# Kernel tuning notes

Measured on AMD Instinct MI355X. Metric: run time of the kernel, lower is better.

The kernel has to match this reference:

```python
import jax, jax.numpy as jnp
import numpy as np

N_NODES = 50000
N_EDGES = 1600000
SLOPE = 0.01  # torch leaky_relu default negative_slope


def _lrelu(x):
    return jnp.where(x >= 0, x, SLOPE * x)


def _graph_conv(x, edge_index, w_rel, b_rel, w_root):
    # PyG GraphConv (aggr='add'): out_i = W_rel @ sum_{j->i} x_j + b_rel + W_root @ x_i
    src, dst = edge_index[0], edge_index[1]
    agg = jax.ops.segment_sum(x[src], dst, num_segments=x.shape[0])  # [N, F_in]
    return agg @ w_rel.T + b_rel + x @ w_root.T


def setup_inputs() -> dict:
    key = jax.random.key(0)
    ks = jax.random.split(key, 12)

    def glorot(k, shape):
        fan_in = shape[-1]
        return jax.random.normal(k, shape, dtype=jnp.float32) / np.sqrt(fan_in)

    x = jax.random.normal(ks[0], (N_NODES, 2048), dtype=jnp.float32)
    edge_index = jax.random.randint(ks[1], (2, N_EDGES), 0, N_NODES, dtype=jnp.int64)

    return {
        "x": x,
        "edge_index": edge_index,
        "lin1_w": glorot(ks[2], (128, 2048)),
        "lin1_b": jnp.zeros((128,), jnp.float32),
        "conv1_w_rel": glorot(ks[3], (64, 128)),
        "conv1_b_rel": jnp.zeros((64,), jnp.float32),
        "conv1_w_root": glorot(ks[4], (64, 128)),
        "conv4_w_rel": glorot(ks[5], (32, 64)),
        "conv4_b_rel": jnp.zeros((32,), jnp.float32),
        "conv4_w_root": glorot(ks[6], (32, 64)),
        "pos_w": glorot(ks[7], (3, 32)),
        "pos_b": jnp.zeros((3,), jnp.float32),
    }


def reference(x, edge_index, lin1_w, lin1_b, conv1_w_rel, conv1_b_rel,
              conv1_w_root, conv4_w_rel, conv4_b_rel, conv4_w_root,
              pos_w, pos_b):
    # dropout layers are identity at inference
    h = _lrelu(x @ lin1_w.T + lin1_b)                                  # [N, 128]
    h = _lrelu(_graph_conv(h, edge_index, conv1_w_rel, conv1_b_rel, conv1_w_root))  # [N, 64]
    h = _lrelu(_graph_conv(h, edge_index, conv4_w_rel, conv4_b_rel, conv4_w_root))  # [N, 32]
    position = h @ pos_w.T + pos_b                                     # [N, 3]
    return position
```

## Files before the change

kernel.cpp:

```cpp
#include <hip/hip_runtime.h>

#define N_NODES 50000
#define N_EDGES 1600000

typedef __attribute__((ext_vector_type(4))) float f32x4;
typedef __attribute__((ext_vector_type(8))) short bf16x8;
typedef unsigned short u16;

__device__ __forceinline__ float lrelu(float x) { return x >= 0.f ? x : 0.01f * x; }

__device__ __forceinline__ u16 f2bf(float f) {
    union { float f; unsigned u; } v; v.f = f;
    unsigned u = v.u;
    u += 0x7fffu + ((u >> 16) & 1u);
    return (u16)(u >> 16);
}

__device__ __forceinline__ float bf2f(u16 v) {
    union { unsigned u; float f; } x; x.u = ((unsigned)v) << 16; return x.f;
}

__device__ __forceinline__ bf16x8 cvt8(float4 a, float4 b) {
    bf16x8 r;
    r[0] = (short)f2bf(a.x); r[1] = (short)f2bf(a.y);
    r[2] = (short)f2bf(a.z); r[3] = (short)f2bf(a.w);
    r[4] = (short)f2bf(b.x); r[5] = (short)f2bf(b.y);
    r[6] = (short)f2bf(b.z); r[7] = (short)f2bf(b.w);
    return r;
}

__device__ __forceinline__ void gload_lds16(const void* g, void* l) {
    __builtin_amdgcn_global_load_lds(
        (const __attribute__((address_space(1))) void*)g,
        (__attribute__((address_space(3))) void*)l, 16, 0, 0);
}

__launch_bounds__(256)
__global__ void k_wprep1(const float* __restrict__ W, u16* __restrict__ Wf)
{
    int i = blockIdx.x * 256 + threadIdx.x;
    int e = i & 7, lane = (i >> 3) & 63, nf = (i >> 9) & 7, ks = i >> 12;
    int n = nf * 16 + (lane & 15);
    int k = ks * 32 + 8 * (lane >> 4) + e;
    Wf[i] = f2bf(W[(size_t)n * 2048 + k]);
}

__launch_bounds__(256)
__global__ void k_wprep2(const float* __restrict__ Wrel, const float* __restrict__ Wroot,
                         u16* __restrict__ Wf)
{
    int i = blockIdx.x * 256 + threadIdx.x;
    int e = i & 7, lane = (i >> 3) & 63, nf = (i >> 9) & 7, ks = i >> 12;
    int n = nf * 16 + (lane & 15);
    int k = ks * 32 + 8 * (lane >> 4) + e;
    float v = (n < 64) ? Wrel[(size_t)n * 128 + k] : Wroot[(size_t)(n - 64) * 128 + k];
    Wf[i] = f2bf(v);
}

__launch_bounds__(256)
__global__ void k_wprep3(const float* __restrict__ Wrel, const float* __restrict__ Wroot,
                         u16* __restrict__ Wf)
{
    int i = blockIdx.x * 256 + threadIdx.x;
    int e = i & 7, lane = (i >> 3) & 63, nf = (i >> 9) & 3, ks = i >> 11;
    int n = nf * 16 + (lane & 15);
    int k = ks * 32 + 8 * (lane >> 4) + e;
    float v = (n < 32) ? Wrel[(size_t)n * 64 + k] : Wroot[(size_t)(n - 32) * 64 + k];
    Wf[i] = f2bf(v);
}

__device__ __forceinline__ void stage_lin1(const float* __restrict__ X,
                                           const u16* __restrict__ Wf,
                                           char* Abuf, char* Bbuf,
                                           int m0, int s, int t)
{
    const int wave = t >> 6;
#pragma unroll
    for (int r = 0; r < 4; r++) {
        int row = r * 16 + (t >> 4);
        int grow = m0 + row; if (grow >= N_NODES) grow = 0;
        int bcol = ((t & 15) * 16) ^ ((row & 7) << 5);
        const float* src = X + (size_t)grow * 2048 + s * 64 + (bcol >> 2);
        gload_lds16(src, Abuf + r * 4096 + wave * 1024);
    }
#pragma unroll
    for (int r = 0; r < 4; r++) {
        const u16* src = Wf + (size_t)s * 8192 + ((size_t)(r * 256 + t)) * 8;
        gload_lds16(src, Bbuf + r * 4096 + wave * 1024);
    }
}

__launch_bounds__(256, 2)
__global__ void k_lin1s(const float* __restrict__ X, const u16* __restrict__ Wf,
                        const float* __restrict__ Bv, u16* __restrict__ H)
{
    __shared__ __align__(16) char As[2][16384];
    __shared__ __align__(16) char Bs[2][16384];

    const int t = threadIdx.x, wave = t >> 6, lane = t & 63;
    const int lrow = lane & 15, lgrp = lane >> 4;
    const int m0 = blockIdx.x * 64;
    const int myrow = wave * 16 + lrow;

    f32x4 acc[8];
#pragma unroll
    for (int i = 0; i < 8; i++) acc[i] = (f32x4)0.f;

    stage_lin1(X, Wf, As[0], Bs[0], m0, 0, t);
    __syncthreads();

    for (int s = 0; s < 32; s++) {
        const int cur = s & 1;
        if (s < 31) stage_lin1(X, Wf, As[cur ^ 1], Bs[cur ^ 1], m0, s + 1, t);

#pragma unroll
        for (int ksub = 0; ksub < 2; ksub++) {
            const int xr = (ksub * 128 + lgrp * 32) ^ ((myrow & 7) << 5);
            const float4* ar = (const float4*)(As[cur] + myrow * 256 + xr);
            float4 a0 = ar[0], a1 = ar[1];
            bf16x8 af = cvt8(a0, a1);
            const char* bb = Bs[cur] + ksub * 8192 + lane * 16;
#pragma unroll
            for (int nf = 0; nf < 8; nf++) {
                bf16x8 bf = *(const bf16x8*)(bb + nf * 1024);
                acc[nf] = __builtin_amdgcn_mfma_f32_16x16x32_bf16(af, bf, acc[nf], 0, 0, 0);
            }
        }
        __syncthreads();
    }

    const int rbase = m0 + wave * 16 + lgrp * 4;
#pragma unroll
    for (int nf = 0; nf < 8; nf++) {
        const int col = nf * 16 + lrow;
        const float bias = Bv[col];
#pragma unroll
        for (int r = 0; r < 4; r++) {
            const int row = rbase + r;
            if (row < N_NODES)
                H[(size_t)row * 128 + col] = f2bf(lrelu(acc[nf][r] + bias));
        }
    }
}

__launch_bounds__(256, 2)
__global__ void k_dualf1(const u16* __restrict__ Hb, const u16* __restrict__ Wf,
                         const float* __restrict__ brel,
                         u16* __restrict__ t1, float* __restrict__ acc1)
{
    const int t = threadIdx.x, wave = t >> 6, lane = t & 63;
    const int lrow = lane & 15, lgrp = lane >> 4;
    const int arow = blockIdx.x * 64 + wave * 16 + lrow;
    const u16* ap = Hb + (size_t)(arow < N_NODES ? arow : 0) * 128 + 8 * lgrp;
    const u16* bp = Wf + lane * 8;

    f32x4 acc[8];
#pragma unroll
    for (int i = 0; i < 8; i++) acc[i] = (f32x4)0.f;

    bf16x8 a0 = *(const bf16x8*)(ap + 0);
    bf16x8 a1 = *(const bf16x8*)(ap + 32);
    bf16x8 a2 = *(const bf16x8*)(ap + 64);
    bf16x8 a3 = *(const bf16x8*)(ap + 96);
    bf16x8 af[4] = {a0, a1, a2, a3};

#pragma unroll
    for (int ks = 0; ks < 4; ks++) {
        const u16* b = bp + ks * 4096;
        bf16x8 a = af[ks];
#pragma unroll
        for (int nf = 0; nf < 8; nf++) {
            bf16x8 bf = *(const bf16x8*)(b + nf * 512);
            acc[nf] = __builtin_amdgcn_mfma_f32_16x16x32_bf16(a, bf, acc[nf], 0, 0, 0);
        }
    }

    const int rbase = blockIdx.x * 64 + wave * 16 + lgrp * 4;
#pragma unroll
    for (int nf = 0; nf < 8; nf++) {
        const int col = nf * 16 + lrow;
#pragma unroll
        for (int r = 0; r < 4; r++) {
            const int row = rbase + r;
            if (row < N_NODES) {
                if (col < 64) t1[(size_t)row * 64 + col] = f2bf(acc[nf][r]);
                else          acc1[(size_t)row * 64 + (col - 64)] = acc[nf][r] + brel[col - 64];
            }
        }
    }
}

__launch_bounds__(256, 2)
__global__ void k_dualf2(const float* __restrict__ A, const u16* __restrict__ Wf,
                         const float* __restrict__ brel,
                         u16* __restrict__ t2, float* __restrict__ acc2)
{
    const int t = threadIdx.x, wave = t >> 6, lane = t & 63;
    const int lrow = lane & 15, lgrp = lane >> 4;
    const int arow = blockIdx.x * 64 + wave * 16 + lrow;
    const float* ap = A + (size_t)(arow < N_NODES ? arow : 0) * 64 + 8 * lgrp;
    const u16* bp = Wf + lane * 8;

    float4 a00 = *(const float4*)(ap + 0);
    float4 a01 = *(const float4*)(ap + 4);
    float4 a10 = *(const float4*)(ap + 32);
    float4 a11 = *(const float4*)(ap + 36);

    f32x4 acc[4];
#pragma unroll
    for (int i = 0; i < 4; i++) acc[i] = (f32x4)0.f;

    a00.x = lrelu(a00.x); a00.y = lrelu(a00.y); a00.z = lrelu(a00.z); a00.w = lrelu(a00.w);
    a01.x = lrelu(a01.x); a01.y = lrelu(a01.y); a01.z = lrelu(a01.z); a01.w = lrelu(a01.w);
    bf16x8 af0 = cvt8(a00, a01);
    a10.x = lrelu(a10.x); a10.y = lrelu(a10.y); a10.z = lrelu(a10.z); a10.w = lrelu(a10.w);
    a11.x = lrelu(a11.x); a11.y = lrelu(a11.y); a11.z = lrelu(a11.z); a11.w = lrelu(a11.w);
    bf16x8 af1 = cvt8(a10, a11);

#pragma unroll
    for (int nf = 0; nf < 4; nf++) {
        bf16x8 b0 = *(const bf16x8*)(bp + nf * 512);
        bf16x8 b1 = *(const bf16x8*)(bp + 2048 + nf * 512);
        acc[nf] = __builtin_amdgcn_mfma_f32_16x16x32_bf16(af0, b0, acc[nf], 0, 0, 0);
        acc[nf] = __builtin_amdgcn_mfma_f32_16x16x32_bf16(af1, b1, acc[nf], 0, 0, 0);
    }

    const int rbase = blockIdx.x * 64 + wave * 16 + lgrp * 4;
#pragma unroll
    for (int nf = 0; nf < 4; nf++) {
        const int col = nf * 16 + lrow;
#pragma unroll
        for (int r = 0; r < 4; r++) {
            const int row = rbase + r;
            if (row < N_NODES) {
                if (col < 32) t2[(size_t)row * 32 + col] = f2bf(acc[nf][r]);
                else          acc2[(size_t)row * 32 + (col - 32)] = acc[nf][r] + brel[col - 32];
            }
        }
    }
}

__launch_bounds__(256)
__global__ void k_zero(int* __restrict__ p, int n)
{
    int i = blockIdx.x * 256 + threadIdx.x;
    if (i < n) p[i] = 0;
}

__launch_bounds__(256)
__global__ void k_hist(const int* __restrict__ ei, int* __restrict__ deg)
{
    const int stride = gridDim.x * 256;
    for (int e = blockIdx.x * 256 + threadIdx.x; e < N_EDGES; e += stride)
        atomicAdd(deg + ei[N_EDGES + e], 1);
}

__launch_bounds__(256)
__global__ void k_scan1(const int* __restrict__ deg, int* __restrict__ tmp,
                        int* __restrict__ bsum)
{
    __shared__ int sm[256];
    const int tid = threadIdx.x;
    const int i = blockIdx.x * 256 + tid;
    int d = (i < N_NODES) ? deg[i] : 0;
    sm[tid] = d;
    __syncthreads();
#pragma unroll
    for (int off = 1; off < 256; off <<= 1) {
        int v = (tid >= off) ? sm[tid - off] : 0;
        __syncthreads();
        sm[tid] += v;
        __syncthreads();
    }
    if (i < N_NODES) tmp[i] = sm[tid];
    if (tid == 255) bsum[blockIdx.x] = sm[255];
}

__launch_bounds__(256)
__global__ void k_scan2p(const int* __restrict__ bsum, int* __restrict__ boff, int nb)
{
    __shared__ int sm[256];
    const int tid = threadIdx.x;
    int v = (tid < nb) ? bsum[tid] : 0;
    sm[tid] = v;
    __syncthreads();
#pragma unroll
    for (int off = 1; off < 256; off <<= 1) {
        int u = (tid >= off) ? sm[tid - off] : 0;
        __syncthreads();
        sm[tid] += u;
        __syncthreads();
    }
    if (tid < nb) boff[tid] = sm[tid] - v;
}

__launch_bounds__(256)
__global__ void k_scan3(const int* __restrict__ tmp, const int* __restrict__ boff,
                        const int* __restrict__ deg, int* __restrict__ ro,
                        int* __restrict__ cur)
{
    const int i = blockIdx.x * 256 + threadIdx.x;
    if (i < N_NODES) {
        int incl = tmp[i] + boff[i >> 8];
        ro[i + 1] = incl;
        cur[i] = incl - deg[i];
    }
    if (i == 0) ro[0] = 0;
}

__launch_bounds__(256)
__global__ void k_fill(const int* __restrict__ ei, int* __restrict__ cur,
                       int* __restrict__ csr)
{
    const int stride = gridDim.x * 256;
    for (int e = blockIdx.x * 256 + threadIdx.x; e < N_EDGES; e += stride) {
        const int dst = ei[N_EDGES + e];
        const int p = atomicAdd(cur + dst, 1);
        csr[p] = ei[e];
    }
}

__launch_bounds__(256)
__global__ void k_gather64(const int* __restrict__ ro, const int* __restrict__ csr,
                           const u16* __restrict__ t, float* __restrict__ acc)
{
    const int wid = (blockIdx.x << 2) | (threadIdx.x >> 6);
    if (wid >= N_NODES) return;
    const int lane = threadIdx.x & 63;
    const int s = ro[wid], e = ro[wid + 1];
    float a = acc[(size_t)wid * 64 + lane];
    int i = s;
    for (; i + 8 <= e; i += 8) {
        int s0 = csr[i], s1 = csr[i + 1], s2 = csr[i + 2], s3 = csr[i + 3];
        int s4 = csr[i + 4], s5 = csr[i + 5], s6 = csr[i + 6], s7 = csr[i + 7];
        u16 v0 = t[(size_t)s0 * 64 + lane], v1 = t[(size_t)s1 * 64 + lane];
        u16 v2 = t[(size_t)s2 * 64 + lane], v3 = t[(size_t)s3 * 64 + lane];
        u16 v4 = t[(size_t)s4 * 64 + lane], v5 = t[(size_t)s5 * 64 + lane];
        u16 v6 = t[(size_t)s6 * 64 + lane], v7 = t[(size_t)s7 * 64 + lane];
        a += bf2f(v0); a += bf2f(v1); a += bf2f(v2); a += bf2f(v3);
        a += bf2f(v4); a += bf2f(v5); a += bf2f(v6); a += bf2f(v7);
    }
    for (; i < e; ++i) a += bf2f(t[(size_t)csr[i] * 64 + lane]);
    acc[(size_t)wid * 64 + lane] = a;
}

__launch_bounds__(256)
__global__ void k_gpos(const int* __restrict__ ro, const int* __restrict__ csr,
                       const u16* __restrict__ t, const float* __restrict__ acc2,
                       const float* __restrict__ PW, const float* __restrict__ PB,
                       float* __restrict__ out)
{
    const int wid = (blockIdx.x << 2) | (threadIdx.x >> 6);
    if (wid >= N_NODES) return;
    const int lane = threadIdx.x & 63;
    const int half = lane >> 5, f = lane & 31;
    const int s = ro[wid], e = ro[wid + 1];
    float a = 0.f;
    int i = s;
    for (; i + 8 <= e; i += 8) {
        int s0 = csr[i + half], s1 = csr[i + 2 + half];
        int s2 = csr[i + 4 + half], s3 = csr[i + 6 + half];
        u16 v0 = t[(size_t)s0 * 32 + f], v1 = t[(size_t)s1 * 32 + f];
        u16 v2 = t[(size_t)s2 * 32 + f], v3 = t[(size_t)s3 * 32 + f];
        a += bf2f(v0); a += bf2f(v1); a += bf2f(v2); a += bf2f(v3);
    }
    for (; i < e; i += 2) {
        int idx = i + half;
        if (idx < e) a += bf2f(t[(size_t)csr[idx] * 32 + f]);
    }
    a += __shfl_xor(a, 32, 64);

    float v = lrelu(acc2[(size_t)wid * 32 + f] + a);
    float p0 = v * PW[f], p1 = v * PW[32 + f], p2 = v * PW[64 + f];
#pragma unroll
    for (int off = 16; off >= 1; off >>= 1) {
        p0 += __shfl_xor(p0, off, 64);
        p1 += __shfl_xor(p1, off, 64);
        p2 += __shfl_xor(p2, off, 64);
    }
    if (lane == 0) {
        out[(size_t)wid * 3 + 0] = p0 + PB[0];
        out[(size_t)wid * 3 + 1] = p1 + PB[1];
        out[(size_t)wid * 3 + 2] = p2 + PB[2];
    }
}

extern "C" void kernel_launch(void* const* d_in, const int* in_sizes, int n_in,
                              void* d_out, int out_size, void* d_ws, size_t ws_size,
                              hipStream_t stream)
{
    const float* x        = (const float*)d_in[0];
    const int*   ei       = (const int*)d_in[1];
    const float* lin1_w   = (const float*)d_in[2];
    const float* lin1_b   = (const float*)d_in[3];
    const float* c1_wrel  = (const float*)d_in[4];
    const float* c1_brel  = (const float*)d_in[5];
    const float* c1_wroot = (const float*)d_in[6];
    const float* c4_wrel  = (const float*)d_in[7];
    const float* c4_brel  = (const float*)d_in[8];
    const float* c4_wroot = (const float*)d_in[9];
    const float* pos_w    = (const float*)d_in[10];
    const float* pos_b    = (const float*)d_in[11];
    float* out = (float*)d_out;

    char* base = (char*)d_ws;
    u16*   h1b  = (u16*)base;
    u16*   t1b  = (u16*)(base + 12800000);
    float* acc1 = (float*)(base + 12800000 + 6400000);
    u16*   t2b  = (u16*)(base + 32000000);
    float* acc2 = (float*)(base + 35200000);
    u16*   wf1  = (u16*)(base + 41600000);
    u16*   wf2  = wf1 + 262144;
    u16*   wf3  = wf2 + 16384;
    int*   ibase = (int*)(wf3 + 4096);
    const int NPAD = ((N_NODES + 255) / 256) * 256;
    int* deg  = ibase;
    int* tmp  = deg  + NPAD;
    int* ro   = tmp  + NPAD;
    int* cur  = ro   + NPAD;
    int* bsum = cur  + NPAD;
    int* boff = bsum + 256;
    int* csr  = boff + 256;
    const int NB = (N_NODES + 255) / 256;

    hipLaunchKernelGGL(k_wprep1, dim3(1024), dim3(256), 0, stream, lin1_w, wf1);
    hipLaunchKernelGGL(k_wprep2, dim3(64), dim3(256), 0, stream, c1_wrel, c1_wroot, wf2);
    hipLaunchKernelGGL(k_wprep3, dim3(16), dim3(256), 0, stream, c4_wrel, c4_wroot, wf3);

    hipLaunchKernelGGL(k_zero, dim3(NB), dim3(256), 0, stream, deg, N_NODES);
    hipLaunchKernelGGL(k_hist, dim3(2048), dim3(256), 0, stream, ei, deg);
    hipLaunchKernelGGL(k_scan1, dim3(NB), dim3(256), 0, stream, deg, tmp, bsum);
    hipLaunchKernelGGL(k_scan2p, dim3(1), dim3(256), 0, stream, bsum, boff, NB);
    hipLaunchKernelGGL(k_scan3, dim3(NB), dim3(256), 0, stream, tmp, boff, deg, ro, cur);
    hipLaunchKernelGGL(k_fill, dim3(2048), dim3(256), 0, stream, ei, cur, csr);

    hipLaunchKernelGGL(k_lin1s, dim3((N_NODES + 63) / 64), dim3(256), 0, stream,
                       x, wf1, lin1_b, h1b);
    hipLaunchKernelGGL(k_dualf1, dim3((N_NODES + 63) / 64), dim3(256), 0, stream,
                       h1b, wf2, c1_brel, t1b, acc1);
    hipLaunchKernelGGL(k_gather64, dim3((N_NODES + 3) / 4), dim3(256), 0, stream,
                       ro, csr, t1b, acc1);
    hipLaunchKernelGGL(k_dualf2, dim3((N_NODES + 63) / 64), dim3(256), 0, stream,
                       acc1, wf3, c4_brel, t2b, acc2);
    hipLaunchKernelGGL(k_gpos, dim3((N_NODES + 3) / 4), dim3(256), 0, stream,
                       ro, csr, t2b, acc2, pos_w, pos_b, out);
}
```

Baseline: 448.6 us.

## Deepen lin1 GEMM pipeline, split conv1 gather into feature halves, merge weight prep

The lin1 GEMM moves from a double-buffered loop over 64-wide K steps to a four-slot ring of 32-wide K steps. It uses explicit vmcnt waits so several global-to-LDS loads stay in flight during MFMA work. The conv1 message tensor is stored as two 32-feature halves, and the gather runs twice, once per half, with two edges handled per wave and a cross-half shuffle reduction. This shrinks each pass's random-access working set to improve cache hits, at the cost of a second pass over the CSR indices. The three weight-prep kernels are merged into one launch to cut launch overhead.

Result: slower. 470.7 us (+4.9%).

```diff
diff --git a/kernel.cpp b/kernel.cpp
--- a/kernel.cpp
+++ b/kernel.cpp
@@ -36,98 +36,111 @@
 }
 
 __launch_bounds__(256)
-__global__ void k_wprep1(const float* __restrict__ W, u16* __restrict__ Wf)
-{
-    int i = blockIdx.x * 256 + threadIdx.x;
-    int e = i & 7, lane = (i >> 3) & 63, nf = (i >> 9) & 7, ks = i >> 12;
-    int n = nf * 16 + (lane & 15);
-    int k = ks * 32 + 8 * (lane >> 4) + e;
-    Wf[i] = f2bf(W[(size_t)n * 2048 + k]);
-}
-
-__launch_bounds__(256)
-__global__ void k_wprep2(const float* __restrict__ Wrel, const float* __restrict__ Wroot,
-                         u16* __restrict__ Wf)
-{
-    int i = blockIdx.x * 256 + threadIdx.x;
-    int e = i & 7, lane = (i >> 3) & 63, nf = (i >> 9) & 7, ks = i >> 12;
-    int n = nf * 16 + (lane & 15);
-    int k = ks * 32 + 8 * (lane >> 4) + e;
-    float v = (n < 64) ? Wrel[(size_t)n * 128 + k] : Wroot[(size_t)(n - 64) * 128 + k];
-    Wf[i] = f2bf(v);
-}
-
-__launch_bounds__(256)
-__global__ void k_wprep3(const float* __restrict__ Wrel, const float* __restrict__ Wroot,
-                         u16* __restrict__ Wf)
-{
-    int i = blockIdx.x * 256 + threadIdx.x;
-    int e = i & 7, lane = (i >> 3) & 63, nf = (i >> 9) & 3, ks = i >> 11;
-    int n = nf * 16 + (lane & 15);
-    int k = ks * 32 + 8 * (lane >> 4) + e;
-    float v = (n < 32) ? Wrel[(size_t)n * 64 + k] : Wroot[(size_t)(n - 32) * 64 + k];
-    Wf[i] = f2bf(v);
-}
-
-__device__ __forceinline__ void stage_lin1(const float* __restrict__ X,
+__global__ void k_wprep(const float* __restrict__ W1,
+                        const float* __restrict__ W2a, const float* __restrict__ W2b,
+                        const float* __restrict__ W3a, const float* __restrict__ W3b,
+                        u16* __restrict__ wf1, u16* __restrict__ wf2, u16* __restrict__ wf3)
+{
+    const int b = blockIdx.x;
+    if (b < 1024) {
+        int i = b * 256 + threadIdx.x;
+        int e = i & 7, lane = (i >> 3) & 63, nf = (i >> 9) & 7, ks = i >> 12;
+        int n = nf * 16 + (lane & 15);
+        int k = ks * 32 + 8 * (lane >> 4) + e;
+        wf1[i] = f2bf(W1[(size_t)n * 2048 + k]);
+    } else if (b < 1088) {
+        int i = (b - 1024) * 256 + threadIdx.x;
+        int e = i & 7, lane = (i >> 3) & 63, nf = (i >> 9) & 7, ks = i >> 12;
+        int n = nf * 16 + (lane & 15);
+        int k = ks * 32 + 8 * (lane >> 4) + e;
+        float v = (n < 64) ? W2a[(size_t)n * 128 + k] : W2b[(size_t)(n - 64) * 128 + k];
+        wf2[i] = f2bf(v);
+    } else {
+        int i = (b - 1088) * 256 + threadIdx.x;
+        int e = i & 7, lane = (i >> 3) & 63, nf = (i >> 9) & 3, ks = i >> 11;
+        int n = nf * 16 + (lane & 15);
+        int k = ks * 32 + 8 * (lane >> 4) + e;
+        float v = (n < 32) ? W3a[(size_t)n * 64 + k] : W3b[(size_t)(n - 32) * 64 + k];
+        wf3[i] = f2bf(v);
+    }
+}
+
+__device__ __forceinline__ void stage_step(const float* __restrict__ X,
                                            const u16* __restrict__ Wf,
-                                           char* Abuf, char* Bbuf,
-                                           int m0, int s, int t)
-{
-    const int wave = t >> 6;
-#pragma unroll
-    for (int r = 0; r < 4; r++) {
-        int row = r * 16 + (t >> 4);
-        int grow = m0 + row; if (grow >= N_NODES) grow = 0;
-        int bcol = ((t & 15) * 16) ^ ((row & 7) << 5);
-        const float* src = X + (size_t)grow * 2048 + s * 64 + (bcol >> 2);
-        gload_lds16(src, Abuf + r * 4096 + wave * 1024);
-    }
-#pragma unroll
-    for (int r = 0; r < 4; r++) {
-        const u16* src = Wf + (size_t)s * 8192 + ((size_t)(r * 256 + t)) * 8;
-        gload_lds16(src, Bbuf + r * 4096 + wave * 1024);
+                                           char* slot, int m0, int s, int t)
+{
+    const int wave = t >> 6, l = t & 63;
+    const int j = l >> 3, g = l & 7;
+#pragma unroll
+    for (int r = 0; r < 2; r++) {
+        int lrow = r * 32 + wave * 8 + j;
+        int grow = m0 + lrow; if (grow >= N_NODES) grow = N_NODES - 1;
+        const float* srcA = X + (size_t)grow * 2048 + s * 32 + (((g ^ j) * 16) >> 2);
+        gload_lds16(srcA, slot + r * 4096 + wave * 1024);
+    }
+#pragma unroll
+    for (int r = 0; r < 2; r++) {
+        const u16* srcB = Wf + (size_t)s * 4096 + (size_t)(r * 256 + t) * 8;
+        gload_lds16(srcB, slot + 8192 + r * 4096 + wave * 1024);
+    }
+}
+
+__device__ __forceinline__ void compute_step(const char* slot, int lane, int wave,
+                                             f32x4 acc[8])
+{
+    const int lrow = lane & 15, lgrp = lane >> 4;
+    const int row = wave * 16 + lrow;
+    const int swz = (row & 7) << 4;
+    const char* Ab = slot + row * 128;
+    float4 a0 = *(const float4*)(Ab + ((lgrp * 32) ^ swz));
+    float4 a1 = *(const float4*)(Ab + ((lgrp * 32 + 16) ^ swz));
+    bf16x8 af = cvt8(a0, a1);
+    const char* Bb = slot + 8192 + lane * 16;
+#pragma unroll
+    for (int nf = 0; nf < 8; nf++) {
+        bf16x8 bf = *(const bf16x8*)(Bb + nf * 1024);
+        acc[nf] = __builtin_amdgcn_mfma_f32_16x16x32_bf16(af, bf, acc[nf], 0, 0, 0);
     }
 }
 
 __launch_bounds__(256, 2)
-__global__ void k_lin1s(const float* __restrict__ X, const u16* __restrict__ Wf,
+__global__ void k_lin1p(const float* __restrict__ X, const u16* __restrict__ Wf,
                         const float* __restrict__ Bv, u16* __restrict__ H)
 {
-    __shared__ __align__(16) char As[2][16384];
-    __shared__ __align__(16) char Bs[2][16384];
-
+    __shared__ __align__(16) char lds[4][16384];
     const int t = threadIdx.x, wave = t >> 6, lane = t & 63;
     const int lrow = lane & 15, lgrp = lane >> 4;
     const int m0 = blockIdx.x * 64;
-    const int myrow = wave * 16 + lrow;
 
     f32x4 acc[8];
 #pragma unroll
     for (int i = 0; i < 8; i++) acc[i] = (f32x4)0.f;
 
-    stage_lin1(X, Wf, As[0], Bs[0], m0, 0, t);
-    __syncthreads();
-
-    for (int s = 0; s < 32; s++) {
-        const int cur = s & 1;
-        if (s < 31) stage_lin1(X, Wf, As[cur ^ 1], Bs[cur ^ 1], m0, s + 1, t);
-
-#pragma unroll
-        for (int ksub = 0; ksub < 2; ksub++) {
-            const int xr = (ksub * 128 + lgrp * 32) ^ ((myrow & 7) << 5);
-            const float4* ar = (const float4*)(As[cur] + myrow * 256 + xr);
-            float4 a0 = ar[0], a1 = ar[1];
-            bf16x8 af = cvt8(a0, a1);
-            const char* bb = Bs[cur] + ksub * 8192 + lane * 16;
-#pragma unroll
-            for (int nf = 0; nf < 8; nf++) {
-                bf16x8 bf = *(const bf16x8*)(bb + nf * 1024);
-                acc[nf] = __builtin_amdgcn_mfma_f32_16x16x32_bf16(af, bf, acc[nf], 0, 0, 0);
-            }
-        }
-        __syncthreads();
-    }
+#pragma unroll
+    for (int s = 0; s < 4; s++) stage_step(X, Wf, lds[s], m0, s, t);
+
+    for (int s = 0; s < 60; s++) {
+        asm volatile("s_waitcnt vmcnt(12)" ::: "memory");
+        __builtin_amdgcn_s_barrier();
+        compute_step(lds[s & 3], lane, wave, acc);
+        __builtin_amdgcn_s_barrier();
+        stage_step(X, Wf, lds[s & 3], m0, s + 4, t);
+    }
+    asm volatile("s_waitcnt vmcnt(12)" ::: "memory");
+    __builtin_amdgcn_s_barrier();
+    compute_step(lds[0], lane, wave, acc);
+    __builtin_amdgcn_s_barrier();
+    asm volatile("s_waitcnt vmcnt(8)" ::: "memory");
+    __builtin_amdgcn_s_barrier();
+    compute_step(lds[1], lane, wave, acc);
+    __builtin_amdgcn_s_barrier();
+    asm volatile("s_waitcnt vmcnt(4)" ::: "memory");
+    __builtin_amdgcn_s_barrier();
+    compute_step(lds[2], lane, wave, acc);
+    __builtin_amdgcn_s_barrier();
+    asm volatile("s_waitcnt vmcnt(0)" ::: "memory");
+    __builtin_amdgcn_s_barrier();
+    compute_step(lds[3], lane, wave, acc);
 
     const int rbase = m0 + wave * 16 + lgrp * 4;
 #pragma unroll
@@ -146,7 +159,7 @@
 __launch_bounds__(256, 2)
 __global__ void k_dualf1(const u16* __restrict__ Hb, const u16* __restrict__ Wf,
                          const float* __restrict__ brel,
-                         u16* __restrict__ t1, float* __restrict__ acc1)
+                         u16* __restrict__ t1h, float* __restrict__ acc1)
 {
     const int t = threadIdx.x, wave = t >> 6, lane = t & 63;
     const int lrow = lane & 15, lgrp = lane >> 4;
@@ -183,8 +196,12 @@
         for (int r = 0; r < 4; r++) {
             const int row = rbase + r;
             if (row < N_NODES) {
-                if (col < 64) t1[(size_t)row * 64 + col] = f2bf(acc[nf][r]);
-                else          acc1[(size_t)row * 64 + (col - 64)] = acc[nf][r] + brel[col - 64];
+                if (col < 64) {
+                    int h = col >> 5;
+                    t1h[(size_t)h * N_NODES * 32 + (size_t)row * 32 + (col & 31)] = f2bf(acc[nf][r]);
+                } else {
+                    acc1[(size_t)row * 64 + (col - 64)] = acc[nf][r] + brel[col - 64];
+                }
             }
         }
     }
@@ -321,27 +338,29 @@
 }
 
 __launch_bounds__(256)
-__global__ void k_gather64(const int* __restrict__ ro, const int* __restrict__ csr,
-                           const u16* __restrict__ t, float* __restrict__ acc)
+__global__ void k_gath64h(const int* __restrict__ ro, const int* __restrict__ csr,
+                          const u16* __restrict__ th, float* __restrict__ acc, int hsel)
 {
     const int wid = (blockIdx.x << 2) | (threadIdx.x >> 6);
     if (wid >= N_NODES) return;
     const int lane = threadIdx.x & 63;
+    const int half = lane >> 5, f = lane & 31;
     const int s = ro[wid], e = ro[wid + 1];
-    float a = acc[(size_t)wid * 64 + lane];
+    float a = 0.f;
     int i = s;
     for (; i + 8 <= e; i += 8) {
-        int s0 = csr[i], s1 = csr[i + 1], s2 = csr[i + 2], s3 = csr[i + 3];
-        int s4 = csr[i + 4], s5 = csr[i + 5], s6 = csr[i + 6], s7 = csr[i + 7];
-        u16 v0 = t[(size_t)s0 * 64 + lane], v1 = t[(size_t)s1 * 64 + lane];
-        u16 v2 = t[(size_t)s2 * 64 + lane], v3 = t[(size_t)s3 * 64 + lane];
-        u16 v4 = t[(size_t)s4 * 64 + lane], v5 = t[(size_t)s5 * 64 + lane];
-        u16 v6 = t[(size_t)s6 * 64 + lane], v7 = t[(size_t)s7 * 64 + lane];
+        int s0 = csr[i + half], s1 = csr[i + 2 + half];
+        int s2 = csr[i + 4 + half], s3 = csr[i + 6 + half];
+        u16 v0 = th[(size_t)s0 * 32 + f], v1 = th[(size_t)s1 * 32 + f];
+        u16 v2 = th[(size_t)s2 * 32 + f], v3 = th[(size_t)s3 * 32 + f];
         a += bf2f(v0); a += bf2f(v1); a += bf2f(v2); a += bf2f(v3);
-        a += bf2f(v4); a += bf2f(v5); a += bf2f(v6); a += bf2f(v7);
-    }
-    for (; i < e; ++i) a += bf2f(t[(size_t)csr[i] * 64 + lane]);
-    acc[(size_t)wid * 64 + lane] = a;
+    }
+    for (; i < e; i += 2) {
+        int idx = i + half;
+        if (idx < e) a += bf2f(th[(size_t)csr[idx] * 32 + f]);
+    }
+    a += __shfl_xor(a, 32, 64);
+    if (half == 0) acc[(size_t)wid * 64 + hsel * 32 + f] += a;
 }
 
 __launch_bounds__(256)
@@ -405,7 +424,7 @@
 
     char* base = (char*)d_ws;
     u16*   h1b  = (u16*)base;
-    u16*   t1b  = (u16*)(base + 12800000);
+    u16*   t1h  = (u16*)(base + 12800000);
     float* acc1 = (float*)(base + 12800000 + 6400000);
     u16*   t2b  = (u16*)(base + 32000000);
     float* acc2 = (float*)(base + 35200000);
@@ -423,9 +442,8 @@
     int* csr  = boff + 256;
     const int NB = (N_NODES + 255) / 256;
 
-    hipLaunchKernelGGL(k_wprep1, dim3(1024), dim3(256), 0, stream, lin1_w, wf1);
-    hipLaunchKernelGGL(k_wprep2, dim3(64), dim3(256), 0, stream, c1_wrel, c1_wroot, wf2);
-    hipLaunchKernelGGL(k_wprep3, dim3(16), dim3(256), 0, stream, c4_wrel, c4_wroot, wf3);
+    hipLaunchKernelGGL(k_wprep, dim3(1104), dim3(256), 0, stream,
+                       lin1_w, c1_wrel, c1_wroot, c4_wrel, c4_wroot, wf1, wf2, wf3);
 
     hipLaunchKernelGGL(k_zero, dim3(NB), dim3(256), 0, stream, deg, N_NODES);
     hipLaunchKernelGGL(k_hist, dim3(2048), dim3(256), 0, stream, ei, deg);
@@ -434,12 +452,14 @@
     hipLaunchKernelGGL(k_scan3, dim3(NB), dim3(256), 0, stream, tmp, boff, deg, ro, cur);
     hipLaunchKernelGGL(k_fill, dim3(2048), dim3(256), 0, stream, ei, cur, csr);
 
-    hipLaunchKernelGGL(k_lin1s, dim3((N_NODES + 63) / 64), dim3(256), 0, stream,
+    hipLaunchKernelGGL(k_lin1p, dim3((N_NODES + 63) / 64), dim3(256), 0, stream,
                        x, wf1, lin1_b, h1b);
     hipLaunchKernelGGL(k_dualf1, dim3((N_NODES + 63) / 64), dim3(256), 0, stream,
-                       h1b, wf2, c1_brel, t1b, acc1);
-    hipLaunchKernelGGL(k_gather64, dim3((N_NODES + 3) / 4), dim3(256), 0, stream,
-                       ro, csr, t1b, acc1);
+                       h1b, wf2, c1_brel, t1h, acc1);
+    hipLaunchKernelGGL(k_gath64h, dim3((N_NODES + 3) / 4), dim3(256), 0, stream,
+                       ro, csr, t1h, acc1, 0);
+    hipLaunchKernelGGL(k_gath64h, dim3((N_NODES + 3) / 4), dim3(256), 0, stream,
+                       ro, csr, t1h + (size_t)N_NODES * 32, acc1, 1);
     hipLaunchKernelGGL(k_dualf2, dim3((N_NODES + 63) / 64), dim3(256), 0, stream,
                        acc1, wf3, c4_brel, t2b, acc2);
     hipLaunchKernelGGL(k_gpos, dim3((N_NODES + 3) / 4), dim3(256), 0, stream,
```
